# Kernel optimization log

Hardware: AMD Instinct MI355X
Metric: run time of the kernel (lower is better)

## Reference

```python
import jax, jax.numpy as jnp
import numpy as np

B, T, M, F, N, H = 2, 1024, 1024, 1024, 16, 64
NEG = -1e30


def _relative_shift(x):
    # x: [b, n, q_len, k_len] -> Transformer-XL pad/reshape shift
    b, h, q_len, k_len = x.shape
    x = jnp.pad(x, ((0, 0), (0, 0), (0, 0), (1, 0)))
    x = x.reshape(b, h, k_len + 1, q_len)[:, :, 1:, :]
    return x.reshape(b, h, q_len, k_len)


def setup_inputs() -> dict:
    key = jax.random.key(0)
    ks = jax.random.split(key, 10)
    std = 0.02
    x = jax.random.normal(ks[0], (B, T, F), jnp.float32)
    rel = jax.random.normal(ks[1], (M + T, F), jnp.float32)
    memory = jax.random.normal(ks[2], (B, M, F), jnp.float32)
    episode_idx = jnp.sort(jax.random.randint(ks[3], (B, M), 0, 4), axis=-1).astype(jnp.int32)
    dones = jax.random.randint(ks[4], (B, T), 0, 2).astype(jnp.int32)
    Wq = jax.random.normal(ks[5], (F, N, H), jnp.float32) * std
    Wk = jax.random.normal(ks[6], (F, N, H), jnp.float32) * std
    Wv = jax.random.normal(ks[7], (F, N, H), jnp.float32) * std
    Wr = jax.random.normal(ks[8], (F, N, H), jnp.float32) * std
    u = jnp.zeros((N, H), jnp.float32)  # bias_init = zeros
    v = jnp.zeros((N, H), jnp.float32)
    Wout = jax.random.normal(ks[9], (N * H, F), jnp.float32) * std
    b_out = jnp.zeros((F,), jnp.float32)
    return {"x": x, "relative_positional_embeddings": rel, "memory": memory,
            "episode_idx": episode_idx, "dones": dones,
            "Wq": Wq, "Wk": Wk, "Wv": Wv, "Wr": Wr, "u": u, "v": v,
            "Wout": Wout, "b_out": b_out}


def reference(x, relative_positional_embeddings, memory, episode_idx, dones,
              Wq, Wk, Wv, Wr, u, v, Wout, b_out):
    scale = 1.0 / np.sqrt(H).astype(np.float32)
    # projections (no bias)
    q = jnp.einsum('btf,fnh->btnh', x, Wq)                      # [B,T,N,H]
    kv_in = jnp.concatenate([memory, x], axis=1)                # [B,M+T,F]
    k = jnp.einsum('bsf,fnh->bsnh', kv_in, Wk)                  # [B,M+T,N,H]
    val = jnp.einsum('bsf,fnh->bsnh', kv_in, Wv)                # [B,M+T,N,H]
    r = jnp.einsum('mf,fnh->mnh', relative_positional_embeddings, Wr)  # [M+T,N,H]

    q_u = q + u[None, None]
    q_v = q + v[None, None]

    # relative positional bias with TXL shift: [B,N,T,M+T]
    bd = jnp.einsum('btnh,mnh->bntm', q_v, r)
    bd = _relative_shift(bd)[..., -(M + T):]
    bias = bd * scale                                           # float32

    # episode mask + causal mask
    qi = episode_idx[:, -1:] + jnp.cumsum(dones, axis=1)        # [B,T]
    ki = jnp.concatenate([episode_idx, qi], axis=1)             # [B,M+T]
    ep_mask = qi[:, None, :, None] == ki[:, None, None, :]      # [B,1,T,M+T]
    causal = jnp.tril(jnp.ones((M + T, M + T), jnp.bool_))[-T:, :][None, None]
    mask = ep_mask & causal                                     # [B,1,T,M+T]

    # attention (matches jax.nn.dot_product_attention XLA path in bf16)
    logits = jnp.einsum('btnh,bsnh->bnts', q_u.astype(jnp.bfloat16), k.astype(jnp.bfloat16))
    logits = logits.astype(jnp.float32) * scale + bias          # [B,N,T,M+T]
    logits = jnp.where(mask, logits, NEG)
    probs = jax.nn.softmax(logits, axis=-1).astype(jnp.bfloat16)
    attn = jnp.einsum('bnts,bsnh->btnh', probs, val.astype(jnp.bfloat16))
    attn = attn.reshape(B, T, N * H).astype(jnp.float32)

    return attn @ Wout + b_out
```

## Files before the change

### kernel.cpp

```cpp
#include <hip/hip_runtime.h>
#include <cstdint>
#include <cstddef>

#define NB 2
#define TT 1024
#define MMEM 1024
#define SS 2048
#define FF 1024
#define NHD 16
#define HD 64

typedef __attribute__((ext_vector_type(8))) short bf16x8;
typedef __attribute__((ext_vector_type(4))) float f32x4;

__device__ __forceinline__ float bf2f(short s){
  unsigned u = ((unsigned)(unsigned short)s) << 16;
  float f; __builtin_memcpy(&f, &u, 4); return f;
}
__device__ __forceinline__ short f2bf(float f){
  unsigned u; __builtin_memcpy(&u, &f, 4);
  u += 0x7fffu + ((u >> 16) & 1u);
  return (short)(u >> 16);
}

typedef const __attribute__((address_space(1))) void gv_t;
typedef __attribute__((address_space(3))) void lv_t;
__device__ __forceinline__ void stage16(const void* g, void* l){
  __builtin_amdgcn_global_load_lds((gv_t*)g, (lv_t*)l, 16, 0, 0);
}


__global__ void cast_kernel(const float* __restrict__ in, short* __restrict__ out, int n4){
  int i = blockIdx.x * blockDim.x + threadIdx.x;
  if (i >= n4) return;
  float4 v = ((const float4*)in)[i];
  short4 o; o.x = f2bf(v.x); o.y = f2bf(v.y); o.z = f2bf(v.z); o.w = f2bf(v.w);
  ((short4*)out)[i] = o;
}

__global__ void build_kv(const float* __restrict__ mem, const float* __restrict__ x,
                         short* __restrict__ out){
  int i = blockIdx.x * blockDim.x + threadIdx.x;
  int idx = i * 4;
  int row = idx >> 10;
  int col = idx & 1023;
  int b = row >> 11, s = row & 2047;
  const float* src = (s < MMEM) ? (mem + ((size_t)b*MMEM + s)*FF + col)
                                : (x   + ((size_t)b*TT + (s - MMEM))*FF + col);
  float4 v = *(const float4*)src;
  short4 o; o.x = f2bf(v.x); o.y = f2bf(v.y); o.z = f2bf(v.z); o.w = f2bf(v.w);
  ((short4*)out)[i] = o;
}

__global__ void transpose_cast5(const float* __restrict__ i0, const float* __restrict__ i1,
                                const float* __restrict__ i2, const float* __restrict__ i3,
                                const float* __restrict__ i4,
                                short* __restrict__ o0, short* __restrict__ o1,
                                short* __restrict__ o2, short* __restrict__ o3,
                                short* __restrict__ o4){
  const float* in; short* out;
  switch (blockIdx.z){
    case 0: in = i0; out = o0; break;
    case 1: in = i1; out = o1; break;
    case 2: in = i2; out = o2; break;
    case 3: in = i3; out = o3; break;
    default: in = i4; out = o4; break;
  }
  __shared__ float tile[32][33];
  int bx = blockIdx.x * 32, by = blockIdx.y * 32;
  int tx = threadIdx.x, ty = threadIdx.y;
  for (int j = ty; j < 32; j += 8)
    tile[j][tx] = in[(size_t)(by + j)*1024 + bx + tx];
  __syncthreads();
  for (int j = ty; j < 32; j += 8)
    out[(size_t)(bx + j)*1024 + by + tx] = f2bf(tile[tx][j]);
}

__global__ void scan_kernel(const int* __restrict__ episode_idx, const int* __restrict__ dones,
                            int* __restrict__ ki, int2* __restrict__ ranges){
  __shared__ int buf[TT];
  __shared__ int kis[SS];
  int b = blockIdx.x, t = threadIdx.x;
  buf[t] = dones[b*TT + t];
  kis[t] = episode_idx[b*MMEM + t];
  __syncthreads();
  for (int off = 1; off < TT; off <<= 1){
    int v = (t >= off) ? buf[t - off] : 0;
    __syncthreads();
    buf[t] += v;
    __syncthreads();
  }
  int base = kis[MMEM - 1];
  int q = base + buf[t];
  kis[MMEM + t] = q;
  ki[b*SS + t] = kis[t];
  ki[b*SS + MMEM + t] = q;
  __syncthreads();
  if (t < 64){
    const int qlo = kis[MMEM + t*16];
    const int qhi = kis[MMEM + t*16 + 15];
    int lo = 0, hi = SS;
    while (lo < hi){ int mid = (lo + hi) >> 1; if (kis[mid] < qlo) lo = mid + 1; else hi = mid; }
    const int s_lo = lo;
    lo = 0; hi = SS;
    const int tgt = qhi + 1;
    while (lo < hi){ int mid = (lo + hi) >> 1; if (kis[mid] < tgt) lo = mid + 1; else hi = mid; }
    int s_hi = lo;
    const int cap = t*16 + 15 + MMEM + 1;
    if (s_hi > cap) s_hi = cap;
    ranges[(b << 6) + t] = make_int2(s_lo, s_hi);
  }
}

__global__ void bias_tables(const short* __restrict__ kbf, const short* __restrict__ rbf,
                            const float* __restrict__ u, const float* __restrict__ v,
                            float* __restrict__ uk, float* __restrict__ vr){
  int i = blockIdx.x * blockDim.x + threadIdx.x;
  if (i < NB * NHD * SS){
    int s = i & 2047, n = (i >> 11) & 15, b = i >> 15;
    const short* kp = kbf + (size_t)(b * SS + s) * 1024 + n * 64;
    const float* up = u + n * 64;
    float acc = 0.f;
    #pragma unroll 8
    for (int h = 0; h < 64; h++) acc += bf2f(kp[h]) * up[h];
    uk[(size_t)(b * NHD + n) * SS + s] = acc;
  } else {
    int j = i - NB * NHD * SS;
    if (j >= NHD * SS) return;
    int jj = j & 2047, n = j >> 11;
    const short* rp = rbf + (size_t)jj * 1024 + n * 64;
    const float* vp = v + n * 64;
    float acc = 0.f;
    #pragma unroll 8
    for (int h = 0; h < 64; h++) acc += bf2f(rp[h]) * vp[h];
    vr[(size_t)n * SS + jj] = acc;
  }
}

__device__ __forceinline__ void gemm_core_128x64(const short* __restrict__ A,
                                                 const short* __restrict__ BT,
                                                 int row0, int col0,
                                                 short* As, short* Bs,
                                                 f32x4 (&acc)[4][2]){
  const int lane = threadIdx.x & 63, wv = threadIdx.x >> 6;
  const int lcol = lane & 15, quad = lane >> 4;
  const int wr = (wv >> 1) * 64, wc = (wv & 1) * 32;
  const int sw = lcol & 7;
  const int ch0 = (quad ^ sw) * 8;
  const int ch1 = ((4 + quad) ^ sw) * 8;

  #pragma unroll
  for (int r = 0; r < 4; r++)
    #pragma unroll
    for (int c = 0; c < 2; c++) acc[r][c] = (f32x4){0.f, 0.f, 0.f, 0.f};

  const short* gA[4]; short* dA[4];
  #pragma unroll
  for (int c = 0; c < 4; c++){
    const int u = (wv * 4 + c) * 64 + lane;
    const int row = u >> 3;
    const int chk = (u & 7) ^ (row & 7);
    gA[c] = A + (size_t)(row0 + row) * 1024 + chk * 8;
    dA[c] = As + (wv * 4 + c) * 512;
  }
  const short* gB[2]; short* dB[2];
  #pragma unroll
  for (int c = 0; c < 2; c++){
    const int u = (wv * 2 + c) * 64 + lane;
    const int row = u >> 3;
    const int chk = (u & 7) ^ (row & 7);
    gB[c] = BT + (size_t)(col0 + row) * 1024 + chk * 8;
    dB[c] = Bs + (wv * 2 + c) * 512;
  }

  #pragma unroll 1
  for (int k0 = 0; k0 < 1024; k0 += 64){
    __syncthreads();
    #pragma unroll
    for (int c = 0; c < 4; c++) stage16(gA[c] + k0, dA[c]);
    #pragma unroll
    for (int c = 0; c < 2; c++) stage16(gB[c] + k0, dB[c]);
    __syncthreads();
    bf16x8 af[4][2];
    #pragma unroll
    for (int r = 0; r < 4; r++){
      const int rb = (wr + r * 16 + lcol) * 64;
      af[r][0] = *(const bf16x8*)&As[rb + ch0];
      af[r][1] = *(const bf16x8*)&As[rb + ch1];
    }
    #pragma unroll
    for (int c = 0; c < 2; c++){
      const int rb = (wc + c * 16 + lcol) * 64;
      bf16x8 b0 = *(const bf16x8*)&Bs[rb + ch0];
      bf16x8 b1 = *(const bf16x8*)&Bs[rb + ch1];
      #pragma unroll
      for (int r = 0; r < 4; r++){
        acc[r][c] = __builtin_amdgcn_mfma_f32_16x16x32_bf16(af[r][0], b0, acc[r][c], 0, 0, 0);
        acc[r][c] = __builtin_amdgcn_mfma_f32_16x16x32_bf16(af[r][1], b1, acc[r][c], 0, 0, 0);
      }
    }
  }
}

__global__ __launch_bounds__(256) void proj_gemm(
    const short* __restrict__ kv, const short* __restrict__ relb,
    const short* __restrict__ WkT, const short* __restrict__ WvT,
    const short* __restrict__ WqT, const short* __restrict__ WrT,
    short* __restrict__ kbf, short* __restrict__ vT,
    short* __restrict__ qb, short* __restrict__ rbf){
  const int z = blockIdx.z;
  const int bx = blockIdx.x;
  const short* A; const short* BT;
  int row0 = bx * 128, qbb = 0;
  if (z == 0){ A = kv; BT = WkT; }
  else if (z == 1){ A = kv; BT = WvT; }
  else if (z == 2){
    if (bx >= 16) return;
    qbb = bx >> 3;
    A = kv + (size_t)(qbb * SS + MMEM) * 1024;
    row0 = (bx & 7) * 128;
    BT = WqT;
  }
  else { if (bx >= 16) return; A = relb; BT = WrT; }
  const int col0 = blockIdx.y * 64;

  __shared__ __align__(16) short As[128*64];
  __shared__ __align__(16) short Bs[64*64];
  f32x4 acc[4][2];
  gemm_core_128x64(A, BT, row0, col0, As, Bs, acc);

  const int lane = threadIdx.x & 63, wv = threadIdx.x >> 6;
  const int lcol = lane & 15, quad = lane >> 4;
  const int wr = (wv >> 1) * 64, wc = (wv & 1) * 32;
  #pragma unroll
  for (int c = 0; c < 2; c++){
    const int cc = col0 + wc + c*16 + lcol;
    #pragma unroll
    for (int r = 0; r < 4; r++){
      #pragma unroll
      for (int ri = 0; ri < 4; ri++){
        const int rr = row0 + wr + r*16 + quad*4 + ri;
        float val = acc[r][c][ri];
        if (z == 0){
          kbf[(size_t)rr * 1024 + cc] = f2bf(val);
        } else if (z == 1){
          int b = rr >> 11, s = rr & 2047;
          vT[(size_t)(((b << 4) + (cc >> 6)) * 64 + (cc & 63)) * 2048 + s] = f2bf(val);
        } else if (z == 2){
          qb[((size_t)(qbb * TT) + rr) * 1024 + cc] = f2bf(val);
        } else {
          rbf[(size_t)rr * 1024 + cc] = f2bf(val);
        }
      }
    }
  }
}

__global__ __launch_bounds__(256) void out_gemm(const short* __restrict__ A,
                                                const short* __restrict__ BT,
                                                const float* __restrict__ bias,
                                                float* __restrict__ C){
  const int row0 = blockIdx.x * 128, col0 = blockIdx.y * 64;
  __shared__ __align__(16) short As[128*64];
  __shared__ __align__(16) short Bs[64*64];
  f32x4 acc[4][2];
  gemm_core_128x64(A, BT, row0, col0, As, Bs, acc);

  const int lane = threadIdx.x & 63, wv = threadIdx.x >> 6;
  const int lcol = lane & 15, quad = lane >> 4;
  const int wr = (wv >> 1) * 64, wc = (wv & 1) * 32;
  #pragma unroll
  for (int c = 0; c < 2; c++){
    const int cc = col0 + wc + c*16 + lcol;
    const float bb = bias[cc];
    #pragma unroll
    for (int r = 0; r < 4; r++)
      #pragma unroll
      for (int ri = 0; ri < 4; ri++){
        const int rr = row0 + wr + r*16 + quad*4 + ri;
        C[(size_t)rr * 1024 + cc] = acc[r][c][ri] + bb;
      }
  }
}

__global__ __launch_bounds__(64) void attn_kernel(const short* __restrict__ qb,
                            const short* __restrict__ rbf,
                            const short* __restrict__ kk, const short* __restrict__ vT,
                            const int* __restrict__ ki,
                            const float* __restrict__ uk, const float* __restrict__ vr,
                            const int2* __restrict__ ranges,
                            short* __restrict__ attn_out){
  const int blk = blockIdx.x;
  const int xcd = blk & 7;
  const int idx = blk >> 3;
  const int bn  = (xcd << 2) | (idx >> 6);
  const int t16 = (idx & 63) * 16;
  const int n = bn & 15;
  const int b = bn >> 4;
  const int lane = threadIdx.x & 63;
  const int quad = lane >> 4, lcol = lane & 15;

  __shared__ __align__(16) short pb[16 * 72];

  const short* qp = qb + (size_t)(b * TT + t16 + lcol) * 1024 + n * 64 + quad * 8;
  bf16x8 aq0 = *(const bf16x8*)(qp);
  bf16x8 aq1 = *(const bf16x8*)(qp + 32);

  int trow[4], qi_r[4], sl[4];
  bool hi[4];
  #pragma unroll
  for (int r = 0; r < 4; r++){
    trow[r] = t16 + quad * 4 + r;
    qi_r[r] = ki[b * SS + MMEM + trow[r]];
    const int rt = quad * 4 + r;
    const int off = lcol + 15 - rt;
    sl[r] = quad * 16 + (off & 15);
    hi[r] = off >= 16;
  }

  float m_run[4], l_run[4];
  f32x4 o[4];
  #pragma unroll
  for (int r = 0; r < 4; r++){ m_run[r] = -1e30f; l_run[r] = 0.f; }
  #pragma unroll
  for (int c = 0; c < 4; c++) o[c] = (f32x4){0.f, 0.f, 0.f, 0.f};

  const float scale = 0.125f;
  const size_t vt_base = (size_t)((b * NHD + n) * HD);
  const short* rb_head = rbf + n * 64;
  const float* uk_row = uk + (size_t)(b * NHD + n) * SS;
  const float* vr_row = vr + (size_t)n * SS;

  const int2 rg = ranges[(b << 6) + (t16 >> 4)];
  const int kt0 = rg.x >> 6, kt1 = (rg.y - 1) >> 6;

  for (int kt = kt0; kt <= kt1; kt++){
    const int s0 = kt * 64;
    f32x4 sacc[4];
    float ukc[4];
    #pragma unroll
    for (int c = 0; c < 4; c++){
      const short* kp = kk + (size_t)(b * SS + s0 + 16 * c + lcol) * 1024 + n * 64 + quad * 8;
      bf16x8 b0 = *(const bf16x8*)(kp);
      bf16x8 b1 = *(const bf16x8*)(kp + 32);
      f32x4 z = (f32x4){0.f, 0.f, 0.f, 0.f};
      z = __builtin_amdgcn_mfma_f32_16x16x32_bf16(aq0, b0, z, 0, 0, 0);
      z = __builtin_amdgcn_mfma_f32_16x16x32_bf16(aq1, b1, z, 0, 0, 0);
      sacc[c] = z;
      ukc[c] = uk_row[s0 + 16 * c + lcol];
    }
    int ki_c[4];
    #pragma unroll
    for (int c = 0; c < 4; c++) ki_c[c] = ki[b * SS + s0 + 16 * c + lcol];

    const int j0 = s0 - t16 + 1008;
    f32x4 Dw[5];
    #pragma unroll
    for (int c5 = 0; c5 < 5; c5++){
      int jr = j0 + 16 * c5 + lcol;
      jr = (jr > SS - 1) ? (SS - 1) : jr;
      const short* rp = rb_head + (size_t)jr * 1024 + quad * 8;
      bf16x8 r0 = *(const bf16x8*)(rp);
      bf16x8 r1 = *(const bf16x8*)(rp + 32);
      f32x4 z = (f32x4){0.f, 0.f, 0.f, 0.f};
      z = __builtin_amdgcn_mfma_f32_16x16x32_bf16(aq0, r0, z, 0, 0, 0);
      z = __builtin_amdgcn_mfma_f32_16x16x32_bf16(aq1, r1, z, 0, 0, 0);
      const float vrj = vr_row[jr];
      #pragma unroll
      for (int r = 0; r < 4; r++) z[r] += vrj;
      Dw[c5] = z;
    }

    float p[4][4];
    float rowmax[4];
    #pragma unroll
    for (int r = 0; r < 4; r++) rowmax[r] = -1e30f;
    #pragma unroll
    for (int c = 0; c < 4; c++){
      const int s = s0 + 16 * c + lcol;
      #pragma unroll
      for (int r = 0; r < 4; r++){
        const float v0 = __shfl(Dw[c][r], sl[r], 64);
        const float v1 = __shfl(Dw[c + 1][r], sl[r], 64);
        const float bd = hi[r] ? v1 : v0;
        float lg = (sacc[c][r] + ukc[c] + bd) * scale;
        const bool valid = (s <= trow[r] + MMEM) && (ki_c[c] == qi_r[r]);
        lg = valid ? lg : -1e30f;
        p[c][r] = lg;
        rowmax[r] = fmaxf(rowmax[r], lg);
      }
    }
    #pragma unroll
    for (int r = 0; r < 4; r++){
      float vmx = rowmax[r];
      #pragma unroll
      for (int off = 1; off < 16; off <<= 1) vmx = fmaxf(vmx, __shfl_xor(vmx, off, 64));
      float mnew = fmaxf(m_run[r], vmx);
      float alpha = __expf(m_run[r] - mnew);
      m_run[r] = mnew;
      l_run[r] *= alpha;
      #pragma unroll
      for (int c = 0; c < 4; c++) o[c][r] *= alpha;
    }
    float psum[4] = {0.f, 0.f, 0.f, 0.f};
    #pragma unroll
    for (int c = 0; c < 4; c++)
      #pragma unroll
      for (int r = 0; r < 4; r++){
        float pv = __expf(p[c][r] - m_run[r]);
        p[c][r] = pv;
        psum[r] += pv;
      }
    #pragma unroll
    for (int r = 0; r < 4; r++){
      float vs = psum[r];
      #pragma unroll
      for (int off = 1; off < 16; off <<= 1) vs += __shfl_xor(vs, off, 64);
      l_run[r] += vs;
    }
    #pragma unroll
    for (int c = 0; c < 4; c++)
      #pragma unroll
      for (int r = 0; r < 4; r++)
        pb[(quad * 4 + r) * 72 + 16 * c + lcol] = f2bf(p[c][r]);
    bf16x8 pa0 = *(const bf16x8*)(&pb[lcol * 72 + quad * 8]);
    bf16x8 pa1 = *(const bf16x8*)(&pb[lcol * 72 + 32 + quad * 8]);
    #pragma unroll
    for (int c = 0; c < 4; c++){
      const short* vtp = vT + (vt_base + c * 16 + lcol) * (size_t)SS + s0 + quad * 8;
      bf16x8 bv0 = *(const bf16x8*)(vtp);
      bf16x8 bv1 = *(const bf16x8*)(vtp + 32);
      o[c] = __builtin_amdgcn_mfma_f32_16x16x32_bf16(pa0, bv0, o[c], 0, 0, 0);
      o[c] = __builtin_amdgcn_mfma_f32_16x16x32_bf16(pa1, bv1, o[c], 0, 0, 0);
    }
  }

  #pragma unroll
  for (int r = 0; r < 4; r++){
    const float inv = 1.f / l_run[r];
    const int t = trow[r];
    #pragma unroll
    for (int c = 0; c < 4; c++)
      attn_out[(size_t)(b * TT + t) * 1024 + n * 64 + c * 16 + lcol] = f2bf(o[c][r] * inv);
  }
}

extern "C" void kernel_launch(void* const* d_in, const int* in_sizes, int n_in,
                              void* d_out, int out_size, void* d_ws, size_t ws_size,
                              hipStream_t stream){
  const float* x      = (const float*)d_in[0];
  const float* rel    = (const float*)d_in[1];
  const float* memory = (const float*)d_in[2];
  const int*   episode_idx = (const int*)d_in[3];
  const int*   dones  = (const int*)d_in[4];
  const float* Wq  = (const float*)d_in[5];
  const float* Wk  = (const float*)d_in[6];
  const float* Wv  = (const float*)d_in[7];
  const float* Wr  = (const float*)d_in[8];
  const float* u   = (const float*)d_in[9];
  const float* v   = (const float*)d_in[10];
  const float* Wout  = (const float*)d_in[11];
  const float* b_out = (const float*)d_in[12];
  float* out = (float*)d_out;

  char* ws = (char*)d_ws;
  size_t off = 0;
  auto alloc = [&](size_t bytes) -> char* {
    char* p = ws + off;
    off += (bytes + 255) & ~(size_t)255;
    return p;
  };
  short* kv_bf  = (short*)alloc((size_t)NB * SS * FF * 2);
  short* rel_bf = (short*)alloc((size_t)SS * FF * 2);
  short* WqT    = (short*)alloc((size_t)FF * 1024 * 2);
  short* WkT    = (short*)alloc((size_t)FF * 1024 * 2);
  short* WvT    = (short*)alloc((size_t)FF * 1024 * 2);
  short* WrT    = (short*)alloc((size_t)FF * 1024 * 2);
  short* WoT    = (short*)alloc((size_t)FF * 1024 * 2);
  short* qbuf   = (short*)alloc((size_t)NB * TT * 1024 * 2);
  short* kbf    = (short*)alloc((size_t)NB * SS * 1024 * 2);
  short* vTb    = (short*)alloc((size_t)NB * SS * 1024 * 2);
  short* rbf    = (short*)alloc((size_t)SS * 1024 * 2);
  int*   ki     = (int*)  alloc((size_t)NB * SS * 4);
  int2*  ranges = (int2*) alloc((size_t)NB * 64 * 8);
  float* ukT    = (float*)alloc((size_t)NB * NHD * SS * 4);
  float* vrT    = (float*)alloc((size_t)NHD * SS * 4);
  short* attn   = (short*)alloc((size_t)NB * TT * 1024 * 2);
  (void)ws_size; (void)in_sizes; (void)n_in; (void)out_size;

  cast_kernel<<<(SS*FF/4 + 255)/256, 256, 0, stream>>>(rel, rel_bf, SS*FF/4);
  build_kv<<<(NB*SS*FF/4)/256, 256, 0, stream>>>(memory, x, kv_bf);
  dim3 tb(32, 8), tg5(32, 32, 5);
  transpose_cast5<<<tg5, tb, 0, stream>>>(Wq, Wk, Wv, Wr, Wout, WqT, WkT, WvT, WrT, WoT);
  scan_kernel<<<NB, TT, 0, stream>>>(episode_idx, dones, ki, ranges);

  proj_gemm<<<dim3(32, 16, 4), 256, 0, stream>>>(kv_bf, rel_bf,
                                                 WkT, WvT, WqT, WrT,
                                                 kbf, vTb, qbuf, rbf);

  bias_tables<<<(NB*NHD*SS + NHD*SS + 255)/256, 256, 0, stream>>>(kbf, rbf, u, v, ukT, vrT);

  attn_kernel<<<2048, 64, 0, stream>>>(qbuf, rbf, kbf, vTb, ki, ukT, vrT, ranges, attn);

  out_gemm<<<dim3(16, 16), 256, 0, stream>>>(attn, WoT, b_out, out);
}
```

Measured before the change: 228.3 us.

## Enlarge projection GEMM tile to 256x64, fuse input casts, vectorize bias tables

The projection GEMM now uses a 256x64 tile per block instead of 128x64, halving the grid so each block reuses its B-operand staging over twice as many rows. The two fp32-to-bf16 cast kernels are merged into one launch, and the bias-table dot products read 16-byte vectors instead of scalar elements. The 128x64 core's loop is also reordered to hoist B fragments. The larger tile doubles accumulator registers and LDS use, which can lower occupancy, and the grid shrinks to 512 active z0/z1 blocks.

After: 238.3 us. 1.04x slower.

```diff
diff --git a/kernel.cpp b/kernel.cpp
--- a/kernel.cpp
+++ b/kernel.cpp
@@ -30,26 +30,28 @@
 }
 
 
-__global__ void cast_kernel(const float* __restrict__ in, short* __restrict__ out, int n4){
+__global__ void build_inputs(const float* __restrict__ mem, const float* __restrict__ x,
+                             const float* __restrict__ rel,
+                             short* __restrict__ kv, short* __restrict__ relo){
   int i = blockIdx.x * blockDim.x + threadIdx.x;
-  if (i >= n4) return;
-  float4 v = ((const float4*)in)[i];
-  short4 o; o.x = f2bf(v.x); o.y = f2bf(v.y); o.z = f2bf(v.z); o.w = f2bf(v.w);
-  ((short4*)out)[i] = o;
-}
-
-__global__ void build_kv(const float* __restrict__ mem, const float* __restrict__ x,
-                         short* __restrict__ out){
-  int i = blockIdx.x * blockDim.x + threadIdx.x;
-  int idx = i * 4;
-  int row = idx >> 10;
-  int col = idx & 1023;
-  int b = row >> 11, s = row & 2047;
-  const float* src = (s < MMEM) ? (mem + ((size_t)b*MMEM + s)*FF + col)
-                                : (x   + ((size_t)b*TT + (s - MMEM))*FF + col);
+  const int nkv = NB * SS * FF / 4;
+  const float* src; short* dst;
+  if (i < nkv){
+    int idx = i * 4;
+    int row = idx >> 10, col = idx & 1023;
+    int b = row >> 11, s = row & 2047;
+    src = (s < MMEM) ? (mem + ((size_t)b*MMEM + s)*FF + col)
+                     : (x   + ((size_t)b*TT + (s - MMEM))*FF + col);
+    dst = kv + (size_t)i * 4;
+  } else {
+    int j = i - nkv;
+    if (j >= SS * FF / 4) return;
+    src = rel + (size_t)j * 4;
+    dst = relo + (size_t)j * 4;
+  }
   float4 v = *(const float4*)src;
   short4 o; o.x = f2bf(v.x); o.y = f2bf(v.y); o.z = f2bf(v.z); o.w = f2bf(v.w);
-  ((short4*)out)[i] = o;
+  *(short4*)dst = o;
 }
 
 __global__ void transpose_cast5(const float* __restrict__ i0, const float* __restrict__ i1,
@@ -116,24 +118,84 @@
                             const float* __restrict__ u, const float* __restrict__ v,
                             float* __restrict__ uk, float* __restrict__ vr){
   int i = blockIdx.x * blockDim.x + threadIdx.x;
+  const short* p; const float* w; float* outp;
   if (i < NB * NHD * SS){
     int s = i & 2047, n = (i >> 11) & 15, b = i >> 15;
-    const short* kp = kbf + (size_t)(b * SS + s) * 1024 + n * 64;
-    const float* up = u + n * 64;
-    float acc = 0.f;
-    #pragma unroll 8
-    for (int h = 0; h < 64; h++) acc += bf2f(kp[h]) * up[h];
-    uk[(size_t)(b * NHD + n) * SS + s] = acc;
+    p = kbf + (size_t)(b * SS + s) * 1024 + n * 64;
+    w = u + n * 64;
+    outp = uk + (size_t)(b * NHD + n) * SS + s;
   } else {
     int j = i - NB * NHD * SS;
     if (j >= NHD * SS) return;
     int jj = j & 2047, n = j >> 11;
-    const short* rp = rbf + (size_t)jj * 1024 + n * 64;
-    const float* vp = v + n * 64;
-    float acc = 0.f;
-    #pragma unroll 8
-    for (int h = 0; h < 64; h++) acc += bf2f(rp[h]) * vp[h];
-    vr[(size_t)n * SS + jj] = acc;
+    p = rbf + (size_t)jj * 1024 + n * 64;
+    w = v + n * 64;
+    outp = vr + (size_t)n * SS + jj;
+  }
+  float acc = 0.f;
+  #pragma unroll
+  for (int c = 0; c < 8; c++){
+    bf16x8 kv8 = *(const bf16x8*)(p + c * 8);
+    float4 w0 = *(const float4*)(w + c * 8);
+    float4 w1 = *(const float4*)(w + c * 8 + 4);
+    acc += bf2f(kv8[0])*w0.x + bf2f(kv8[1])*w0.y + bf2f(kv8[2])*w0.z + bf2f(kv8[3])*w0.w
+         + bf2f(kv8[4])*w1.x + bf2f(kv8[5])*w1.y + bf2f(kv8[6])*w1.z + bf2f(kv8[7])*w1.w;
+  }
+  *outp = acc;
+}
+
+__device__ __forceinline__ void gemm_core_256x64(const short* __restrict__ A,
+                                                 const short* __restrict__ BT,
+                                                 int row0, int col0,
+                                                 short* As, short* Bs,
+                                                 f32x4 (&acc)[8][2]){
+  const int tid = threadIdx.x;
+  const int lane = tid & 63, wv = tid >> 6;
+  const int lcol = lane & 15, quad = lane >> 4;
+  const int wr = (wv >> 1) * 128, wc = (wv & 1) * 32;
+  const int sw = lcol & 7;
+  const int ch0 = (quad ^ sw) * 8;
+  const int ch1 = ((4 + quad) ^ sw) * 8;
+
+  #pragma unroll
+  for (int r = 0; r < 8; r++)
+    #pragma unroll
+    for (int c = 0; c < 2; c++) acc[r][c] = (f32x4){0.f, 0.f, 0.f, 0.f};
+
+  const int chk = (tid & 7) ^ ((tid >> 3) & 7);
+  const short* gA0 = A  + (size_t)(row0 + (tid >> 3)) * 1024 + chk * 8;
+  const short* gB0 = BT + (size_t)(col0 + (tid >> 3)) * 1024 + chk * 8;
+  short* dA0 = As + wv * 512;
+  short* dB0 = Bs + wv * 512;
+
+  #pragma unroll 1
+  for (int k0 = 0; k0 < 1024; k0 += 64){
+    __syncthreads();
+    #pragma unroll
+    for (int j = 0; j < 8; j++)
+      stage16(gA0 + (size_t)j * 32768 + k0, dA0 + j * 2048);
+    #pragma unroll
+    for (int j = 0; j < 2; j++)
+      stage16(gB0 + (size_t)j * 32768 + k0, dB0 + j * 2048);
+    __syncthreads();
+    bf16x8 bfr[2][2];
+    #pragma unroll
+    for (int c = 0; c < 2; c++){
+      const int rb = (wc + c * 16 + lcol) * 64;
+      bfr[c][0] = *(const bf16x8*)&Bs[rb + ch0];
+      bfr[c][1] = *(const bf16x8*)&Bs[rb + ch1];
+    }
+    #pragma unroll
+    for (int r = 0; r < 8; r++){
+      const int rb = (wr + r * 16 + lcol) * 64;
+      bf16x8 a0 = *(const bf16x8*)&As[rb + ch0];
+      bf16x8 a1 = *(const bf16x8*)&As[rb + ch1];
+      #pragma unroll
+      for (int c = 0; c < 2; c++){
+        acc[r][c] = __builtin_amdgcn_mfma_f32_16x16x32_bf16(a0, bfr[c][0], acc[r][c], 0, 0, 0);
+        acc[r][c] = __builtin_amdgcn_mfma_f32_16x16x32_bf16(a1, bfr[c][1], acc[r][c], 0, 0, 0);
+      }
+    }
   }
 }
 
@@ -142,7 +204,8 @@
                                                  int row0, int col0,
                                                  short* As, short* Bs,
                                                  f32x4 (&acc)[4][2]){
-  const int lane = threadIdx.x & 63, wv = threadIdx.x >> 6;
+  const int tid = threadIdx.x;
+  const int lane = tid & 63, wv = tid >> 6;
   const int lcol = lane & 15, quad = lane >> 4;
   const int wr = (wv >> 1) * 64, wc = (wv & 1) * 32;
   const int sw = lcol & 7;
@@ -154,49 +217,37 @@
     #pragma unroll
     for (int c = 0; c < 2; c++) acc[r][c] = (f32x4){0.f, 0.f, 0.f, 0.f};
 
-  const short* gA[4]; short* dA[4];
-  #pragma unroll
-  for (int c = 0; c < 4; c++){
-    const int u = (wv * 4 + c) * 64 + lane;
-    const int row = u >> 3;
-    const int chk = (u & 7) ^ (row & 7);
-    gA[c] = A + (size_t)(row0 + row) * 1024 + chk * 8;
-    dA[c] = As + (wv * 4 + c) * 512;
-  }
-  const short* gB[2]; short* dB[2];
-  #pragma unroll
-  for (int c = 0; c < 2; c++){
-    const int u = (wv * 2 + c) * 64 + lane;
-    const int row = u >> 3;
-    const int chk = (u & 7) ^ (row & 7);
-    gB[c] = BT + (size_t)(col0 + row) * 1024 + chk * 8;
-    dB[c] = Bs + (wv * 2 + c) * 512;
-  }
+  const int chk = (tid & 7) ^ ((tid >> 3) & 7);
+  const short* gA0 = A  + (size_t)(row0 + (tid >> 3)) * 1024 + chk * 8;
+  const short* gB0 = BT + (size_t)(col0 + (tid >> 3)) * 1024 + chk * 8;
+  short* dA0 = As + wv * 512;
+  short* dB0 = Bs + wv * 512;
 
   #pragma unroll 1
   for (int k0 = 0; k0 < 1024; k0 += 64){
     __syncthreads();
     #pragma unroll
-    for (int c = 0; c < 4; c++) stage16(gA[c] + k0, dA[c]);
-    #pragma unroll
-    for (int c = 0; c < 2; c++) stage16(gB[c] + k0, dB[c]);
+    for (int j = 0; j < 4; j++)
+      stage16(gA0 + (size_t)j * 32768 + k0, dA0 + j * 2048);
+    stage16(gB0 + k0, dB0);
+    stage16(gB0 + 32768 + k0, dB0 + 2048);
     __syncthreads();
-    bf16x8 af[4][2];
+    bf16x8 bfr[2][2];
+    #pragma unroll
+    for (int c = 0; c < 2; c++){
+      const int rb = (wc + c * 16 + lcol) * 64;
+      bfr[c][0] = *(const bf16x8*)&Bs[rb + ch0];
+      bfr[c][1] = *(const bf16x8*)&Bs[rb + ch1];
+    }
     #pragma unroll
     for (int r = 0; r < 4; r++){
       const int rb = (wr + r * 16 + lcol) * 64;
-      af[r][0] = *(const bf16x8*)&As[rb + ch0];
-      af[r][1] = *(const bf16x8*)&As[rb + ch1];
-    }
-    #pragma unroll
-    for (int c = 0; c < 2; c++){
-      const int rb = (wc + c * 16 + lcol) * 64;
-      bf16x8 b0 = *(const bf16x8*)&Bs[rb + ch0];
-      bf16x8 b1 = *(const bf16x8*)&Bs[rb + ch1];
-      #pragma unroll
-      for (int r = 0; r < 4; r++){
-        acc[r][c] = __builtin_amdgcn_mfma_f32_16x16x32_bf16(af[r][0], b0, acc[r][c], 0, 0, 0);
-        acc[r][c] = __builtin_amdgcn_mfma_f32_16x16x32_bf16(af[r][1], b1, acc[r][c], 0, 0, 0);
+      bf16x8 a0 = *(const bf16x8*)&As[rb + ch0];
+      bf16x8 a1 = *(const bf16x8*)&As[rb + ch1];
+      #pragma unroll
+      for (int c = 0; c < 2; c++){
+        acc[r][c] = __builtin_amdgcn_mfma_f32_16x16x32_bf16(a0, bfr[c][0], acc[r][c], 0, 0, 0);
+        acc[r][c] = __builtin_amdgcn_mfma_f32_16x16x32_bf16(a1, bfr[c][1], acc[r][c], 0, 0, 0);
       }
     }
   }
@@ -211,32 +262,32 @@
   const int z = blockIdx.z;
   const int bx = blockIdx.x;
   const short* A; const short* BT;
-  int row0 = bx * 128, qbb = 0;
+  int row0 = bx * 256, qbb = 0;
   if (z == 0){ A = kv; BT = WkT; }
   else if (z == 1){ A = kv; BT = WvT; }
   else if (z == 2){
-    if (bx >= 16) return;
-    qbb = bx >> 3;
+    if (bx >= 8) return;
+    qbb = bx >> 2;
     A = kv + (size_t)(qbb * SS + MMEM) * 1024;
-    row0 = (bx & 7) * 128;
+    row0 = (bx & 3) * 256;
     BT = WqT;
   }
-  else { if (bx >= 16) return; A = relb; BT = WrT; }
+  else { if (bx >= 8) return; A = relb; BT = WrT; }
   const int col0 = blockIdx.y * 64;
 
-  __shared__ __align__(16) short As[128*64];
+  __shared__ __align__(16) short As[256*64];
   __shared__ __align__(16) short Bs[64*64];
-  f32x4 acc[4][2];
-  gemm_core_128x64(A, BT, row0, col0, As, Bs, acc);
+  f32x4 acc[8][2];
+  gemm_core_256x64(A, BT, row0, col0, As, Bs, acc);
 
   const int lane = threadIdx.x & 63, wv = threadIdx.x >> 6;
   const int lcol = lane & 15, quad = lane >> 4;
-  const int wr = (wv >> 1) * 64, wc = (wv & 1) * 32;
+  const int wr = (wv >> 1) * 128, wc = (wv & 1) * 32;
   #pragma unroll
   for (int c = 0; c < 2; c++){
     const int cc = col0 + wc + c*16 + lcol;
     #pragma unroll
-    for (int r = 0; r < 4; r++){
+    for (int r = 0; r < 8; r++){
       #pragma unroll
       for (int ri = 0; ri < 4; ri++){
         const int rr = row0 + wr + r*16 + quad*4 + ri;
@@ -488,13 +539,13 @@
   short* attn   = (short*)alloc((size_t)NB * TT * 1024 * 2);
   (void)ws_size; (void)in_sizes; (void)n_in; (void)out_size;
 
-  cast_kernel<<<(SS*FF/4 + 255)/256, 256, 0, stream>>>(rel, rel_bf, SS*FF/4);
-  build_kv<<<(NB*SS*FF/4)/256, 256, 0, stream>>>(memory, x, kv_bf);
+  const int n4 = NB*SS*FF/4 + SS*FF/4;
+  build_inputs<<<(n4 + 255)/256, 256, 0, stream>>>(memory, x, rel, kv_bf, rel_bf);
   dim3 tb(32, 8), tg5(32, 32, 5);
   transpose_cast5<<<tg5, tb, 0, stream>>>(Wq, Wk, Wv, Wr, Wout, WqT, WkT, WvT, WrT, WoT);
   scan_kernel<<<NB, TT, 0, stream>>>(episode_idx, dones, ki, ranges);
 
-  proj_gemm<<<dim3(32, 16, 4), 256, 0, stream>>>(kv_bf, rel_bf,
+  proj_gemm<<<dim3(16, 16, 4), 256, 0, stream>>>(kv_bf, rel_bf,
                                                  WkT, WvT, WqT, WrT,
                                                  kbf, vTb, qbuf, rbf);
 
```
